# Kernel optimization log

Measured on AMD Instinct MI355X. Metric: run time of the kernel, lower is better.

Reference implementation:

```python
import jax, jax.numpy as jnp
import numpy as np


def _binarize(x):
    # sign binarize: +1 for x > 0, -1 for x <= 0 (matches torch: ones_like, then -1 where <=0)
    return jnp.where(x <= 0, -1.0, 1.0).astype(x.dtype)


def setup_inputs() -> dict:
    key = jax.random.key(0)
    kx, kw = jax.random.split(key)
    x = jax.random.normal(kx, (32, 256, 56, 56), dtype=jnp.float32)
    weight = jax.random.normal(kw, (256, 256, 3, 3), dtype=jnp.float32) * 0.05
    return {"x": x, "weight": weight}


def reference(x, weight):
    xb = _binarize(x)
    wb = _binarize(weight)
    # NCHW input, OIHW weight; stride 1, padding 1, dilation 1, groups 1
    out = jax.lax.conv_general_dilated(
        xb, wb,
        window_strides=(1, 1),
        padding=((1, 1), (1, 1)),
        rhs_dilation=(1, 1),
        dimension_numbers=("NCHW", "OIHW", "NCHW"),
        feature_group_count=1,
    )
    return out
```

## Files before the change

### kernel.cpp

```cpp
#include <hip/hip_runtime.h>
#include <stdint.h>


#define N_BATCH 32
#define C_IN    256
#define HH      56
#define WW_     56
#define HW      (HH * WW_)
#define C_OUT   256
#define WORDS   8
#define TAPS    9
#define OBLK    8
#define PH      58
#define PW      58

__global__ __launch_bounds__(256) void pack_x_kernel(const float* __restrict__ x,
                                                     uint32_t* __restrict__ xp) {
    int tid = blockIdx.x * 256 + threadIdx.x;
    int s = tid % HW;
    int t = tid / HW;
    int n = t % N_BATCH;
    int word = t / N_BATCH;
    int h = s / WW_, w = s % WW_;
    const float* px = x + ((size_t)(n * C_IN + word * 32)) * HW + s;
    uint32_t bits = 0;
#pragma unroll
    for (int i = 0; i < 32; ++i) {
        float v = px[(size_t)i * HW];
        bits |= (v > 0.0f ? 1u : 0u) << i;
    }
    xp[(((size_t)n * PH + (h + 1)) * PW + (w + 1)) * WORDS + word] = bits;
}

__global__ __launch_bounds__(256) void pack_w_kernel(const float* __restrict__ w,
                                                     uint32_t* __restrict__ wp) {
    int tid = blockIdx.x * 256 + threadIdx.x;
    int o = tid / (TAPS * WORDS);
    int r = tid % (TAPS * WORDS);
    int tap = r / WORDS;
    int j = r % WORDS;
    uint32_t bits = 0;
#pragma unroll
    for (int i = 0; i < 32; ++i) {
        int c = j * 32 + i;
        float v = w[((size_t)(o * C_IN + c)) * TAPS + tap];
        bits |= (v > 0.0f ? 1u : 0u) << i;
    }
    wp[tid] = bits;
}

__global__ void corr_kernel(const uint32_t* __restrict__ wp,
                            uint32_t* __restrict__ corrT) {
    int o = threadIdx.x;
    int pc[TAPS];
#pragma unroll
    for (int tap = 0; tap < TAPS; ++tap) {
        int c = 0;
#pragma unroll
        for (int j = 0; j < WORDS; ++j)
            c += __popc(wp[((size_t)o * TAPS + tap) * WORDS + j]);
        pc[tap] = c;
    }
#pragma unroll
    for (int hp = 0; hp < 3; ++hp) {
#pragma unroll
        for (int wq = 0; wq < 3; ++wq) {
            int nv = (hp == 1 ? 3 : 2) * (wq == 1 ? 3 : 2);
            int sinv = 0;
#pragma unroll
            for (int kh = -1; kh <= 1; ++kh) {
#pragma unroll
                for (int kw = -1; kw <= 1; ++kw) {
                    bool inv = (kh == -1 && hp == 0) || (kh == 1 && hp == 2) ||
                               (kw == -1 && wq == 0) || (kw == 1 && wq == 2);
                    if (inv) sinv += pc[(kh + 1) * 3 + (kw + 1)];
                }
            }
            corrT[(hp * 3 + wq) * C_OUT + o] = (uint32_t)(256 * nv + 2 * sinv);
        }
    }
}

__global__ __launch_bounds__(256) void bconv_kernel(const uint32_t* __restrict__ xp,
                                                    const uint32_t* __restrict__ wp,
                                                    const uint32_t* __restrict__ corrT,
                                                    float* __restrict__ out) {
    int s = blockIdx.x * 256 + threadIdx.x;
    if (s >= HW) return;
    int n = blockIdx.z;
    int o_base = blockIdx.y * OBLK;
    int h = s / WW_;
    int w = s % WW_;

    const uint32_t* base = xp + (((size_t)n * PH + (h + 1)) * PW + (w + 1)) * WORDS;

    int acc[OBLK];
#pragma unroll
    for (int o = 0; o < OBLK; ++o) acc[o] = 0;

#pragma unroll
    for (int kh = -1; kh <= 1; ++kh) {
#pragma unroll
        for (int kw = -1; kw <= 1; ++kw) {
            const uint32_t* px = base + (kh * PW + kw) * WORDS;
            uint4 a = *reinterpret_cast<const uint4*>(px);
            uint4 b = *reinterpret_cast<const uint4*>(px + 4);
            uint32_t xw[8] = {a.x, a.y, a.z, a.w, b.x, b.y, b.z, b.w};
            int tap = (kh + 1) * 3 + (kw + 1);
#pragma unroll
            for (int o = 0; o < OBLK; ++o) {
                const uint32_t* pw = wp + ((size_t)(o_base + o) * TAPS + tap) * WORDS;
#pragma unroll
                for (int j = 0; j < WORDS; ++j) {
                    acc[o] += __popc(xw[j] ^ pw[j]);
                }
            }
        }
    }

    int hp = (h == 0) ? 0 : ((h == HH - 1) ? 2 : 1);
    int wq = (w == 0) ? 0 : ((w == WW_ - 1) ? 2 : 1);
    const uint32_t* ct = corrT + (hp * 3 + wq) * C_OUT + o_base;

#pragma unroll
    for (int o = 0; o < OBLK; ++o) {
        out[((size_t)(n * C_OUT + o_base + o)) * HW + s] =
            (float)((int)ct[o] - 2 * acc[o]);
    }
}

extern "C" void kernel_launch(void* const* d_in, const int* in_sizes, int n_in,
                              void* d_out, int out_size, void* d_ws, size_t ws_size,
                              hipStream_t stream) {
    const float* x = (const float*)d_in[0];
    const float* w = (const float*)d_in[1];
    float* out = (float*)d_out;

    uint32_t* xp    = (uint32_t*)d_ws;
    uint32_t* wp    = xp + (size_t)N_BATCH * PH * PW * WORDS;
    uint32_t* corrT = wp + (size_t)C_OUT * TAPS * WORDS;

    hipMemsetAsync(xp, 0, (size_t)N_BATCH * PH * PW * WORDS * sizeof(uint32_t), stream);

    pack_x_kernel<<<dim3(HW * N_BATCH * WORDS / 256), 256, 0, stream>>>(x, xp);
    pack_w_kernel<<<dim3(C_OUT * TAPS * WORDS / 256), 256, 0, stream>>>(w, wp);
    corr_kernel<<<dim3(1), 256, 0, stream>>>(wp, corrT);

    dim3 grid((HW + 255) / 256, C_OUT / OBLK, N_BATCH);
    bconv_kernel<<<grid, 256, 0, stream>>>(xp, wp, corrT, out);
}
```

Before: 292.9 us.

## Map threads to output channels with register-resident weights and LDS-transposed stores

```diff
diff --git a/kernel.cpp b/kernel.cpp
--- a/kernel.cpp
+++ b/kernel.cpp
@@ -10,9 +10,9 @@
 #define C_OUT   256
 #define WORDS   8
 #define TAPS    9
-#define OBLK    8
 #define PH      58
 #define PW      58
+#define CHUNK   32
 
 __global__ __launch_bounds__(256) void pack_x_kernel(const float* __restrict__ x,
                                                      uint32_t* __restrict__ xp) {
@@ -81,51 +81,73 @@
     }
 }
 
-__global__ __launch_bounds__(256) void bconv_kernel(const uint32_t* __restrict__ xp,
-                                                    const uint32_t* __restrict__ wp,
-                                                    const uint32_t* __restrict__ corrT,
-                                                    float* __restrict__ out) {
-    int s = blockIdx.x * 256 + threadIdx.x;
-    if (s >= HW) return;
-    int n = blockIdx.z;
-    int o_base = blockIdx.y * OBLK;
-    int h = s / WW_;
-    int w = s % WW_;
+__global__ __launch_bounds__(256) void bconv2_kernel(const uint32_t* __restrict__ xp,
+                                                     const uint32_t* __restrict__ wp,
+                                                     const uint32_t* __restrict__ corrT,
+                                                     float* __restrict__ out) {
+    __shared__ float lds[4][16][65];
 
-    const uint32_t* base = xp + (((size_t)n * PH + (h + 1)) * PW + (w + 1)) * WORDS;
+    const int lane = threadIdx.x;
+    const int wv   = threadIdx.y;
+    const int o    = wv * 64 + lane;
+    const int n    = blockIdx.y;
+    const int s0   = blockIdx.x * CHUNK;
 
-    int acc[OBLK];
+    uint32_t wreg[TAPS * WORDS];
+    {
+        const uint4* wpo = reinterpret_cast<const uint4*>(wp + (size_t)o * (TAPS * WORDS));
 #pragma unroll
-    for (int o = 0; o < OBLK; ++o) acc[o] = 0;
+        for (int t = 0; t < 18; ++t)
+            reinterpret_cast<uint4*>(wreg)[t] = wpo[t];
+    }
+    int cc[9];
+#pragma unroll
+    for (int cfg = 0; cfg < 9; ++cfg)
+        cc[cfg] = (int)corrT[cfg * C_OUT + o];
 
 #pragma unroll
-    for (int kh = -1; kh <= 1; ++kh) {
+    for (int g = 0; g < 2; ++g) {
+#pragma unroll 4
+        for (int pi = 0; pi < 16; ++pi) {
+            int s = s0 + g * 16 + pi;
+            int h = s / WW_;
+            int w = s - h * WW_;
+
+            int acc = 0;
 #pragma unroll
-        for (int kw = -1; kw <= 1; ++kw) {
-            const uint32_t* px = base + (kh * PW + kw) * WORDS;
-            uint4 a = *reinterpret_cast<const uint4*>(px);
-            uint4 b = *reinterpret_cast<const uint4*>(px + 4);
-            uint32_t xw[8] = {a.x, a.y, a.z, a.w, b.x, b.y, b.z, b.w};
-            int tap = (kh + 1) * 3 + (kw + 1);
+            for (int r = 0; r < 3; ++r) {
+                const uint32_t* pr = xp + (((size_t)n * PH + h + r) * PW + w) * WORDS;
 #pragma unroll
-            for (int o = 0; o < OBLK; ++o) {
-                const uint32_t* pw = wp + ((size_t)(o_base + o) * TAPS + tap) * WORDS;
+                for (int t = 0; t < 3; ++t) {
 #pragma unroll
-                for (int j = 0; j < WORDS; ++j) {
-                    acc[o] += __popc(xw[j] ^ pw[j]);
+                    for (int j = 0; j < WORDS; ++j)
+                        acc += __popc(pr[t * WORDS + j] ^ wreg[(r * 3 + t) * WORDS + j]);
                 }
             }
+
+            int hp = (h == 0) ? 0 : ((h == HH - 1) ? 2 : 1);
+            int wq = (w == 0) ? 0 : ((w == WW_ - 1) ? 2 : 1);
+            int cfg = hp * 3 + wq;
+            int corrV;
+            switch (cfg) {
+                case 0: corrV = cc[0]; break;
+                case 1: corrV = cc[1]; break;
+                case 2: corrV = cc[2]; break;
+                case 3: corrV = cc[3]; break;
+                case 4: corrV = cc[4]; break;
+                case 5: corrV = cc[5]; break;
+                case 6: corrV = cc[6]; break;
+                case 7: corrV = cc[7]; break;
+                default: corrV = cc[8]; break;
+            }
+            lds[wv][pi][lane] = (float)(corrV - 2 * acc);
         }
-    }
-
-    int hp = (h == 0) ? 0 : ((h == HH - 1) ? 2 : 1);
-    int wq = (w == 0) ? 0 : ((w == WW_ - 1) ? 2 : 1);
-    const uint32_t* ct = corrT + (hp * 3 + wq) * C_OUT + o_base;
-
 #pragma unroll
-    for (int o = 0; o < OBLK; ++o) {
-        out[((size_t)(n * C_OUT + o_base + o)) * HW + s] =
-            (float)((int)ct[o] - 2 * acc[o]);
+        for (int k = 0; k < 16; ++k) {
+            int oo = k * 4 + (lane >> 4);
+            int ss = s0 + g * 16 + (lane & 15);
+            out[((size_t)n * C_OUT + wv * 64 + oo) * HW + ss] = lds[wv][lane & 15][oo];
+        }
     }
 }
 
@@ -146,6 +168,5 @@
     pack_w_kernel<<<dim3(C_OUT * TAPS * WORDS / 256), 256, 0, stream>>>(w, wp);
     corr_kernel<<<dim3(1), 256, 0, stream>>>(wp, corrT);
 
-    dim3 grid((HW + 255) / 256, C_OUT / OBLK, N_BATCH);
-    bconv_kernel<<<grid, 256, 0, stream>>>(xp, wp, corrT, out);
+    bconv2_kernel<<<dim3(HW / CHUNK, N_BATCH), dim3(64, 4), 0, stream>>>(xp, wp, corrT, out);
 }
```

Measured after the change: 380.9 us. 1.3x slower.

## Fuse prep kernels, zero only halo, stage weights in LDS, persistent conv blocks

Applied to the files above, without the earlier changes.

```diff
diff --git a/kernel.cpp b/kernel.cpp
--- a/kernel.cpp
+++ b/kernel.cpp
@@ -10,122 +10,149 @@
 #define C_OUT   256
 #define WORDS   8
 #define TAPS    9
-#define OBLK    8
 #define PH      58
 #define PW      58
+#define GRID_PREP 1024
 
-__global__ __launch_bounds__(256) void pack_x_kernel(const float* __restrict__ x,
-                                                     uint32_t* __restrict__ xp) {
-    int tid = blockIdx.x * 256 + threadIdx.x;
-    int s = tid % HW;
-    int t = tid / HW;
-    int n = t % N_BATCH;
-    int word = t / N_BATCH;
-    int h = s / WW_, w = s % WW_;
-    const float* px = x + ((size_t)(n * C_IN + word * 32)) * HW + s;
-    uint32_t bits = 0;
+__global__ __launch_bounds__(256) void prep_kernel(const float* __restrict__ x,
+                                                   const float* __restrict__ wt,
+                                                   uint32_t* __restrict__ xp,
+                                                   uint32_t* __restrict__ wp) {
+    const int T = GRID_PREP * 256;
+    const int tid0 = blockIdx.x * 256 + threadIdx.x;
+
+    for (int i = tid0; i < N_BATCH * 228 * WORDS; i += T) {
+        int n = i / (228 * WORDS);
+        int r = i % (228 * WORDS);
+        int pos = r / WORDS, word = r % WORDS;
+        int hh, ww;
+        if (pos < 58)       { hh = 0;             ww = pos; }
+        else if (pos < 116) { hh = 57;            ww = pos - 58; }
+        else if (pos < 172) { hh = pos - 116 + 1; ww = 0; }
+        else                { hh = pos - 172 + 1; ww = 57; }
+        xp[(((size_t)n * PH + hh) * PW + ww) * WORDS + word] = 0u;
+    }
+
+    for (int i = tid0; i < C_OUT * TAPS * WORDS; i += T) {
+        int o = i / (TAPS * WORDS);
+        int r = i % (TAPS * WORDS);
+        int tap = r / WORDS, j = r % WORDS;
+        uint32_t bits = 0;
 #pragma unroll
-    for (int i = 0; i < 32; ++i) {
-        float v = px[(size_t)i * HW];
-        bits |= (v > 0.0f ? 1u : 0u) << i;
+        for (int ii = 0; ii < 32; ++ii) {
+            float v = wt[((size_t)(o * C_IN + j * 32 + ii)) * TAPS + tap];
+            bits |= (v > 0.0f ? 1u : 0u) << ii;
+        }
+        wp[i] = bits;
     }
-    xp[(((size_t)n * PH + (h + 1)) * PW + (w + 1)) * WORDS + word] = bits;
-}
 
-__global__ __launch_bounds__(256) void pack_w_kernel(const float* __restrict__ w,
-                                                     uint32_t* __restrict__ wp) {
-    int tid = blockIdx.x * 256 + threadIdx.x;
-    int o = tid / (TAPS * WORDS);
-    int r = tid % (TAPS * WORDS);
-    int tap = r / WORDS;
-    int j = r % WORDS;
-    uint32_t bits = 0;
+    for (int i = tid0; i < N_BATCH * HW * WORDS; i += T) {
+        int s = i % HW;
+        int t = i / HW;
+        int n = t % N_BATCH;
+        int word = t / N_BATCH;
+        int h = s / WW_, w2 = s % WW_;
+        const float* px = x + ((size_t)(n * C_IN + word * 32)) * HW + s;
+        uint32_t bits = 0;
 #pragma unroll
-    for (int i = 0; i < 32; ++i) {
-        int c = j * 32 + i;
-        float v = w[((size_t)(o * C_IN + c)) * TAPS + tap];
-        bits |= (v > 0.0f ? 1u : 0u) << i;
-    }
-    wp[tid] = bits;
-}
-
-__global__ void corr_kernel(const uint32_t* __restrict__ wp,
-                            uint32_t* __restrict__ corrT) {
-    int o = threadIdx.x;
-    int pc[TAPS];
-#pragma unroll
-    for (int tap = 0; tap < TAPS; ++tap) {
-        int c = 0;
-#pragma unroll
-        for (int j = 0; j < WORDS; ++j)
-            c += __popc(wp[((size_t)o * TAPS + tap) * WORDS + j]);
-        pc[tap] = c;
-    }
-#pragma unroll
-    for (int hp = 0; hp < 3; ++hp) {
-#pragma unroll
-        for (int wq = 0; wq < 3; ++wq) {
-            int nv = (hp == 1 ? 3 : 2) * (wq == 1 ? 3 : 2);
-            int sinv = 0;
-#pragma unroll
-            for (int kh = -1; kh <= 1; ++kh) {
-#pragma unroll
-                for (int kw = -1; kw <= 1; ++kw) {
-                    bool inv = (kh == -1 && hp == 0) || (kh == 1 && hp == 2) ||
-                               (kw == -1 && wq == 0) || (kw == 1 && wq == 2);
-                    if (inv) sinv += pc[(kh + 1) * 3 + (kw + 1)];
-                }
-            }
-            corrT[(hp * 3 + wq) * C_OUT + o] = (uint32_t)(256 * nv + 2 * sinv);
+        for (int ii = 0; ii < 32; ++ii) {
+            float v = px[(size_t)ii * HW];
+            bits |= (v > 0.0f ? 1u : 0u) << ii;
         }
+        xp[(((size_t)n * PH + (h + 1)) * PW + (w2 + 1)) * WORDS + word] = bits;
     }
 }
 
-__global__ __launch_bounds__(256) void bconv_kernel(const uint32_t* __restrict__ xp,
-                                                    const uint32_t* __restrict__ wp,
-                                                    const uint32_t* __restrict__ corrT,
-                                                    float* __restrict__ out) {
-    int s = blockIdx.x * 256 + threadIdx.x;
-    if (s >= HW) return;
-    int n = blockIdx.z;
-    int o_base = blockIdx.y * OBLK;
-    int h = s / WW_;
-    int w = s % WW_;
+__global__ __launch_bounds__(256, 4) void bconv3_kernel(const uint32_t* __restrict__ xp,
+                                                        const uint32_t* __restrict__ wp,
+                                                        float* __restrict__ out) {
+    __shared__ __align__(16) uint32_t wlds[8 * TAPS * WORDS];
+    __shared__ int clds[9][8];
 
-    const uint32_t* base = xp + (((size_t)n * PH + (h + 1)) * PW + (w + 1)) * WORDS;
+    const int tid = threadIdx.x;
+    const int b = blockIdx.x;
+    const int n  = (b & 7) * 4 + (b >> 8);
+    const int ob = (b >> 3) & 31;
+    const int o_base = ob * 8;
 
-    int acc[OBLK];
+    if (tid < 144)
+        reinterpret_cast<uint4*>(wlds)[tid] =
+            reinterpret_cast<const uint4*>(wp + (size_t)o_base * TAPS * WORDS)[tid];
+
+    if (tid < 8) {
+        int pc[TAPS];
 #pragma unroll
-    for (int o = 0; o < OBLK; ++o) acc[o] = 0;
-
+        for (int tap = 0; tap < TAPS; ++tap) {
+            int c = 0;
 #pragma unroll
-    for (int kh = -1; kh <= 1; ++kh) {
+            for (int j = 0; j < WORDS; ++j)
+                c += __popc(wp[((size_t)(o_base + tid) * TAPS + tap) * WORDS + j]);
+            pc[tap] = c;
+        }
 #pragma unroll
-        for (int kw = -1; kw <= 1; ++kw) {
-            const uint32_t* px = base + (kh * PW + kw) * WORDS;
-            uint4 a = *reinterpret_cast<const uint4*>(px);
-            uint4 b = *reinterpret_cast<const uint4*>(px + 4);
-            uint32_t xw[8] = {a.x, a.y, a.z, a.w, b.x, b.y, b.z, b.w};
-            int tap = (kh + 1) * 3 + (kw + 1);
+        for (int hp = 0; hp < 3; ++hp) {
 #pragma unroll
-            for (int o = 0; o < OBLK; ++o) {
-                const uint32_t* pw = wp + ((size_t)(o_base + o) * TAPS + tap) * WORDS;
+            for (int wq = 0; wq < 3; ++wq) {
+                int nv = (hp == 1 ? 3 : 2) * (wq == 1 ? 3 : 2);
+                int sinv = 0;
 #pragma unroll
-                for (int j = 0; j < WORDS; ++j) {
-                    acc[o] += __popc(xw[j] ^ pw[j]);
-                }
+                for (int kh = 0; kh < 3; ++kh)
+#pragma unroll
+                    for (int kw = 0; kw < 3; ++kw) {
+                        bool inv = (kh == 0 && hp == 0) || (kh == 2 && hp == 2) ||
+                                   (kw == 0 && wq == 0) || (kw == 2 && wq == 2);
+                        if (inv) sinv += pc[kh * 3 + kw];
+                    }
+                clds[hp * 3 + wq][tid] = 256 * nv + 2 * sinv;
             }
         }
     }
+    __syncthreads();
 
-    int hp = (h == 0) ? 0 : ((h == HH - 1) ? 2 : 1);
-    int wq = (w == 0) ? 0 : ((w == WW_ - 1) ? 2 : 1);
-    const uint32_t* ct = corrT + (hp * 3 + wq) * C_OUT + o_base;
+    const uint32_t* xpn = xp + (size_t)n * PH * PW * WORDS;
+
+#pragma unroll 1
+    for (int chunk = 0; chunk < 13; ++chunk) {
+        int s = chunk * 256 + tid;
+        if (s < HW) {
+            int h = s / WW_;
+            int w2 = s - h * WW_;
+
+            int acc[8];
+#pragma unroll
+            for (int lo = 0; lo < 8; ++lo) acc[lo] = 0;
 
 #pragma unroll
-    for (int o = 0; o < OBLK; ++o) {
-        out[((size_t)(n * C_OUT + o_base + o)) * HW + s] =
-            (float)((int)ct[o] - 2 * acc[o]);
+            for (int r = 0; r < 3; ++r) {
+                const uint32_t* pr = xpn + ((size_t)(h + r) * PW + w2) * WORDS;
+#pragma unroll
+                for (int t = 0; t < 3; ++t) {
+                    uint4 a = *reinterpret_cast<const uint4*>(pr + t * WORDS);
+                    uint4 bq = *reinterpret_cast<const uint4*>(pr + t * WORDS + 4);
+                    uint32_t xw[8] = {a.x, a.y, a.z, a.w, bq.x, bq.y, bq.z, bq.w};
+                    int tap = r * 3 + t;
+#pragma unroll
+                    for (int lo = 0; lo < 8; ++lo) {
+                        const uint32_t* pwl = wlds + (lo * TAPS + tap) * WORDS;
+                        uint4 w0 = *reinterpret_cast<const uint4*>(pwl);
+                        uint4 w1 = *reinterpret_cast<const uint4*>(pwl + 4);
+                        acc[lo] += __popc(xw[0] ^ w0.x) + __popc(xw[1] ^ w0.y) +
+                                   __popc(xw[2] ^ w0.z) + __popc(xw[3] ^ w0.w) +
+                                   __popc(xw[4] ^ w1.x) + __popc(xw[5] ^ w1.y) +
+                                   __popc(xw[6] ^ w1.z) + __popc(xw[7] ^ w1.w);
+                    }
+                }
+            }
+
+            int hp = (h == 0) ? 0 : ((h == HH - 1) ? 2 : 1);
+            int wq = (w2 == 0) ? 0 : ((w2 == WW_ - 1) ? 2 : 1);
+            int cfgb = hp * 3 + wq;
+#pragma unroll
+            for (int lo = 0; lo < 8; ++lo) {
+                out[((size_t)(n * C_OUT + o_base + lo)) * HW + s] =
+                    (float)(clds[cfgb][lo] - 2 * acc[lo]);
+            }
+        }
     }
 }
 
@@ -136,16 +163,9 @@
     const float* w = (const float*)d_in[1];
     float* out = (float*)d_out;
 
-    uint32_t* xp    = (uint32_t*)d_ws;
-    uint32_t* wp    = xp + (size_t)N_BATCH * PH * PW * WORDS;
-    uint32_t* corrT = wp + (size_t)C_OUT * TAPS * WORDS;
+    uint32_t* xp = (uint32_t*)d_ws;
+    uint32_t* wp = xp + (size_t)N_BATCH * PH * PW * WORDS;
 
-    hipMemsetAsync(xp, 0, (size_t)N_BATCH * PH * PW * WORDS * sizeof(uint32_t), stream);
-
-    pack_x_kernel<<<dim3(HW * N_BATCH * WORDS / 256), 256, 0, stream>>>(x, xp);
-    pack_w_kernel<<<dim3(C_OUT * TAPS * WORDS / 256), 256, 0, stream>>>(w, wp);
-    corr_kernel<<<dim3(1), 256, 0, stream>>>(wp, corrT);
-
-    dim3 grid((HW + 255) / 256, C_OUT / OBLK, N_BATCH);
-    bconv_kernel<<<grid, 256, 0, stream>>>(xp, wp, corrT, out);
+    prep_kernel<<<dim3(GRID_PREP), 256, 0, stream>>>(x, w, xp, wp);
+    bconv3_kernel<<<dim3(1024), 256, 0, stream>>>(xp, wp, out);
 }
```

New measurement: 758.5 us. +159.0%, slower.
